# Optimization experiments

Measured on AMD Instinct MI355X. Metric: run time of the kernel, lower is better.

The kernel has to match this reference:

```python
import jax, jax.numpy as jnp
import numpy as np

EPS = 1e-10

def gru_dir(x, Wih, Whh, bih, bhh, reverse=False):
    # x: [B,T,in]; torch GRU gate order r,z,n
    B = x.shape[0]
    H = Whh.shape[1]
    xs = jnp.einsum('bti,gi->btg', x, Wih) + bih  # [B,T,3H] input proj precomputed
    if reverse:
        xs = xs[:, ::-1]
    h0 = jnp.zeros((B, H), x.dtype)
    def step(h, xt):
        gh = h @ Whh.T + bhh
        xr, xz, xn = jnp.split(xt, 3, axis=-1)
        hr, hz, hn = jnp.split(gh, 3, axis=-1)
        r = jax.nn.sigmoid(xr + hr)
        z = jax.nn.sigmoid(xz + hz)
        n = jnp.tanh(xn + r * hn)
        h = (1.0 - z) * n + z * h
        return h, h
    _, ys = jax.lax.scan(step, h0, jnp.swapaxes(xs, 0, 1))
    ys = jnp.swapaxes(ys, 0, 1)
    if reverse:
        ys = ys[:, ::-1]
    return ys

def bigru(x, Wih, Whh, bih, bhh):
    f = gru_dir(x, Wih[0], Whh[0], bih[0], bhh[0], False)
    b = gru_dir(x, Wih[1], Whh[1], bih[1], bhh[1], True)
    return jnp.concatenate([f, b], -1)

def graph_decomp(lab, nb, nb_mask, layers=2):
    # lab: [N,D]; nb: [N,K] neighbor ids; nb_mask: [N,K] 0/1 validity
    m = nb_mask.astype(lab.dtype)
    for _ in range(layers):
        Lj = lab[nb]                                   # [N,K,D]
        x1 = jnp.sum(lab[:, None, :] * Lj, -1)         # <Li,Lj>
        x2 = jnp.sum(Lj * Lj, -1) + EPS                # <Lj,Lj>
        proj = (x1 / x2)[..., None] * Lj               # scaled projection
        deg = jnp.sum(m, -1)                           # [N]
        mean = jnp.sum(proj * m[..., None], 1) / jnp.maximum(deg, 1.0)[:, None]
        lab = jnp.where(deg[:, None] > 0, lab - mean, lab)
    return lab

def code_wise(query, context):
    # query [B,N,D], context [B,T,D] -> [B,1,D]
    S = jnp.einsum('btd,bnd->btn', context, query)
    att = jax.nn.softmax(jnp.max(S, 2), axis=-1)       # [B,T]
    return jnp.einsum('bt,btd->bd', att, context)[:, None, :]

def mask_attention(query, context):
    # query [B,L,D], context [B,T,D] -> [B,T,D]
    att = jnp.einsum('btd,bld->btl', context, query)
    am = jnp.where(att == 0, -jnp.inf, att)
    sm = jax.nn.softmax(am, axis=-1)
    sm = jnp.where(jnp.isnan(sm), 0.0, sm)             # NaN rows (all -inf) -> 0
    return jnp.einsum('btl,bld->btd', sm, query)

def fact_separation(verdict_hidden, circ):
    scenario = mask_attention(verdict_hidden, circ)
    x3 = jnp.sum(circ * scenario, 2)
    x4 = jnp.sum(scenario * scenario, 2) + EPS
    similar = (x3 / x4)[..., None] * scenario
    return similar, circ - similar


def setup_inputs() -> dict:
    key = jax.random.key(0)
    ks = iter(jax.random.split(key, 64))
    def nrm(shape, s=0.1):
        return jax.random.normal(next(ks), shape, jnp.float32) * s
    def ints(shape, hi):
        return jax.random.randint(next(ks), shape, 0, hi)
    V, D, H = 339503, 200, 150
    B, T = 32, 512
    Nc, Na, K = 119, 103, 8
    Lc, La, Lv = 32, 64, 50
    def gru_p(pfx, din, h):
        return {pfx+'_Wih': nrm((2, 3*h, din)), pfx+'_Whh': nrm((2, 3*h, h)),
                pfx+'_bih': nrm((2, 3*h)), pfx+'_bhh': nrm((2, 3*h))}
    inp = {'emb': nrm((V, D), 1.0)}
    inp.update(gru_p('enc', D, H))
    inp.update(gru_p('encch', D, H))
    inp.update(gru_p('term', 6*H, 3*H))
    inp.update(gru_p('art', 8*H, 4*H))
    inp.update({'Wc': nrm((Nc, 6*H)), 'bc': nrm((Nc,)),
                'Wa': nrm((Na, 8*H)), 'ba': nrm((Na,)),
                'Wt': nrm((11, 6*H)), 'bt': nrm((11,))})
    inp.update({'documents': ints((B, T), V),
                'charge_tokens': ints((Nc, Lc), V),
                'article_tokens': ints((Na, La), V),
                'charge_nb': ints((Nc, K), Nc),
                'charge_nb_mask': ints((Nc, K), 2).astype(jnp.int32),
                'article_nb': ints((Na, K), Na),
                'article_nb_mask': ints((Na, K), 2).astype(jnp.int32),
                'verdict_charge_tokens': ints((Nc, Lv), V),
                'verdict_article_tokens': ints((Na, Lv), V)})
    return inp


def reference(emb, enc_Wih, enc_Whh, enc_bih, enc_bhh,
              encch_Wih, encch_Whh, encch_bih, encch_bhh,
              term_Wih, term_Whh, term_bih, term_bhh,
              art_Wih, art_Whh, art_bih, art_bhh,
              Wc, bc, Wa, ba, Wt, bt,
              documents, charge_tokens, article_tokens,
              charge_nb, charge_nb_mask, article_nb, article_nb_mask,
              verdict_charge_tokens, verdict_article_tokens):
    # label encodings (shared encoder_charge)
    ch = bigru(emb[charge_tokens], encch_Wih, encch_Whh, encch_bih, encch_bhh)
    ar = bigru(emb[article_tokens], encch_Wih, encch_Whh, encch_bih, encch_bhh)
    _charge = ch.mean(1); ori_a = _charge                      # [Nc,300]
    _article = ar.mean(1); ori_b = _article                    # [Na,300]
    new_charge = graph_decomp(_charge, charge_nb, charge_nb_mask, 2)
    new_article = graph_decomp(_article, article_nb, article_nb_mask, 2)

    d_hidden = bigru(emb[documents], enc_Wih, enc_Whh, enc_bih, enc_bhh)  # [B,T,300]
    B, T, Dh = d_hidden.shape
    def cw(labels):
        q = jnp.broadcast_to(labels[None], (B,) + labels.shape)
        return code_wise(q, d_hidden)                          # [B,1,300]
    tile = lambda v: jnp.broadcast_to(v, (B, T, Dh))

    d_hc = cw(new_charge); d_a = cw(ori_a)
    fact_charge = jnp.concatenate([d_hidden, tile(d_hc), tile(d_a)], -1)  # [B,T,900]
    charge_out = fact_charge.mean(1) @ Wc.T + bc
    cp = jnp.argmax(charge_out, 1)                             # predicted charge ids
    vch = bigru(emb[verdict_charge_tokens[cp]], enc_Wih, enc_Whh, enc_bih, enc_bhh)
    adc, sec = fact_separation(vch, d_hidden)

    d_ha = cw(new_article); d_b = cw(ori_b)
    fact_article = jnp.concatenate([d_hidden, tile(d_ha), adc, tile(d_b)], -1)  # [B,T,1200]
    fah = bigru(fact_article, art_Wih, art_Whh, art_bih, art_bhh).mean(1)
    article_out = fah @ Wa.T + ba
    ap = jnp.argmax(article_out, 1)
    var = bigru(emb[verdict_article_tokens[ap]], enc_Wih, enc_Whh, enc_bih, enc_bhh)
    ssc, dsc = fact_separation(var, sec)

    term = jnp.concatenate([d_hidden, ssc, dsc], -1)           # [B,T,900]
    th = bigru(term, term_Wih, term_Whh, term_bih, term_bhh).mean(1)
    time_out = th @ Wt.T + bt
    return charge_out, article_out, time_out
```

## Files before the change

kernel.cpp:

```cpp
#include <hip/hip_runtime.h>
#include <hip/hip_bf16.h>

#define DEVI __device__ __forceinline__

DEVI float sigm(float x){ return 1.f/(1.f+expf(-x)); }

typedef int v4i __attribute__((ext_vector_type(4)));
typedef float f4 __attribute__((ext_vector_type(4)));
using bf16x8 = __attribute__((ext_vector_type(8))) short;

DEVI v4i make_srsrc(const void* p, unsigned bytes){
  unsigned long long a = (unsigned long long)p;
  v4i r;
  r.x = (int)(a & 0xFFFFFFFFull);
  r.y = (int)((a >> 32) & 0xFFFFull);
  r.z = (int)bytes;
  r.w = 0x00020000;
  return r;
}

DEVI unsigned packsplit(float a){
  unsigned u = __float_as_uint(a);
  unsigned hi = (u + 0x7fffu + ((u >> 16) & 1u)) & 0xffff0000u;
  float res = a - __uint_as_float(hi);
  unsigned v = __float_as_uint(res);
  unsigned lo = ((v + 0x7fffu + ((v >> 16) & 1u)) >> 16) & 0xffffu;
  return hi | lo;
}

__global__ void k_transpose(const float* __restrict__ in, float* __restrict__ out, int R, int C){
  int b = blockIdx.y;
  long n = (long)R*C;
  long i = (long)blockIdx.x*256 + threadIdx.x;
  if (i < n){
    int r = (int)(i / C), c = (int)(i % C);
    out[(long)b*n + (long)c*R + r] = in[(long)b*n + i];
  }
}

__global__ void k_gather_p(const float* __restrict__ emb, const int* __restrict__ tok, unsigned* __restrict__ out){
  int row = blockIdx.x; int c = threadIdx.x;
  if (c < 200) out[(long)row*200 + c] = packsplit(emb[(long)tok[row]*200 + c]);
}
__global__ void k_gather_sel_p(const float* __restrict__ emb, const int* __restrict__ tok, const int* __restrict__ sel, unsigned* __restrict__ out){
  int t = blockIdx.x, b = blockIdx.y; int c = threadIdx.x;
  if (c < 200){
    int tk = tok[(long)sel[b]*50 + t];
    out[((long)b*50 + t)*200 + c] = packsplit(emb[(long)tk*200 + c]);
  }
}

__global__ void k_packAc(const float* __restrict__ src, unsigned* __restrict__ dst, long n){
  long i = (long)blockIdx.x*256 + threadIdx.x;
  if (i < n) dst[i] = packsplit(src[i]);
}
__global__ void k_packW(const float* __restrict__ src, unsigned* __restrict__ dst, int R, int K, int KP){
  long i = (long)blockIdx.x*256 + threadIdx.x;
  if (i < (long)R*KP){
    int r = (int)(i / KP), k = (int)(i % KP);
    dst[i] = (k < K) ? packsplit(src[(long)r*K + k]) : 0u;
  }
}

__global__ __launch_bounds__(256) void k_gemm_bf3(
    const unsigned* __restrict__ Ap, const unsigned* __restrict__ Wp,
    const float* __restrict__ bias, float* __restrict__ C,
    int M, int N, int K, int KP, long sW, long sC, long sBias)
{
  int dir = blockIdx.z;
  Wp += (long)dir*sW; C += (long)dir*sC;
  if (bias) bias += (long)dir*sBias;
  int n0 = blockIdx.x*128, m0 = blockIdx.y*128;
  __shared__ unsigned short Ah[128*72], Al[128*72], Bh[128*72], Bl[128*72];
  int tid = threadIdx.x;
  int w = tid >> 6, lane = tid & 63;
  int l15 = lane & 15, lg = lane >> 4;
  f4 acc[2][8] = {};

  for (int k0 = 0; k0 < K; k0 += 64){
    __syncthreads();
    for (int u = tid; u < 2048; u += 256){
      int r = u >> 4, q = u & 15;
      int k = k0 + q*4;
      uint4 pa = make_uint4(0,0,0,0);
      if (k + 4 <= K) pa = *(const uint4*)&Ap[(long)(m0 + r)*K + k];
      ushort4 h4, s4;
      h4.x=(unsigned short)(pa.x>>16); s4.x=(unsigned short)(pa.x&0xffff);
      h4.y=(unsigned short)(pa.y>>16); s4.y=(unsigned short)(pa.y&0xffff);
      h4.z=(unsigned short)(pa.z>>16); s4.z=(unsigned short)(pa.z&0xffff);
      h4.w=(unsigned short)(pa.w>>16); s4.w=(unsigned short)(pa.w&0xffff);
      *(ushort4*)&Ah[r*72 + q*4] = h4;
      *(ushort4*)&Al[r*72 + q*4] = s4;
      int n = n0 + r;
      uint4 pw = make_uint4(0,0,0,0);
      if (n < N && k + 4 <= KP) pw = *(const uint4*)&Wp[(long)n*KP + k];
      ushort4 wh, wl;
      wh.x=(unsigned short)(pw.x>>16); wl.x=(unsigned short)(pw.x&0xffff);
      wh.y=(unsigned short)(pw.y>>16); wl.y=(unsigned short)(pw.y&0xffff);
      wh.z=(unsigned short)(pw.z>>16); wl.z=(unsigned short)(pw.z&0xffff);
      wh.w=(unsigned short)(pw.w>>16); wl.w=(unsigned short)(pw.w&0xffff);
      *(ushort4*)&Bh[r*72 + q*4] = wh;
      *(ushort4*)&Bl[r*72 + q*4] = wl;
    }
    __syncthreads();
    bf16x8 ah[2][2], al[2][2];
    #pragma unroll
    for (int fm=0; fm<2; fm++)
      #pragma unroll
      for (int ks=0; ks<2; ks++){
        int idx = (w*32 + fm*16 + l15)*72 + ks*32 + lg*8;
        ah[fm][ks] = *(const bf16x8*)&Ah[idx];
        al[fm][ks] = *(const bf16x8*)&Al[idx];
      }
    #pragma unroll
    for (int fn=0; fn<8; fn++){
      int bidx0 = (fn*16 + l15)*72 + lg*8;
      bf16x8 bh0 = *(const bf16x8*)&Bh[bidx0];
      bf16x8 bh1 = *(const bf16x8*)&Bh[bidx0 + 32];
      bf16x8 bl0 = *(const bf16x8*)&Bl[bidx0];
      bf16x8 bl1 = *(const bf16x8*)&Bl[bidx0 + 32];
      #pragma unroll
      for (int fm=0; fm<2; fm++){
        f4 a = acc[fm][fn];
        a = __builtin_amdgcn_mfma_f32_16x16x32_bf16(ah[fm][0], bh0, a, 0, 0, 0);
        a = __builtin_amdgcn_mfma_f32_16x16x32_bf16(al[fm][0], bh0, a, 0, 0, 0);
        a = __builtin_amdgcn_mfma_f32_16x16x32_bf16(ah[fm][0], bl0, a, 0, 0, 0);
        a = __builtin_amdgcn_mfma_f32_16x16x32_bf16(ah[fm][1], bh1, a, 0, 0, 0);
        a = __builtin_amdgcn_mfma_f32_16x16x32_bf16(al[fm][1], bh1, a, 0, 0, 0);
        a = __builtin_amdgcn_mfma_f32_16x16x32_bf16(ah[fm][1], bl1, a, 0, 0, 0);
        acc[fm][fn] = a;
      }
    }
  }
  #pragma unroll
  for (int fm=0; fm<2; fm++)
    #pragma unroll
    for (int fn=0; fn<8; fn++){
      int row = m0 + w*32 + fm*16 + lg*4;
      int col = n0 + fn*16 + l15;
      if (col < N){
        float bv = bias ? bias[col] : 0.f;
        #pragma unroll
        for (int r2=0; r2<4; r2++)
          if (row + r2 < M)
            C[(long)(row+r2)*N + col] = acc[fm][fn][r2] + bv;
      }
    }
}

__global__ __launch_bounds__(256) void k_gemm128(
    const float* __restrict__ A, const float* __restrict__ W,
    const float* __restrict__ bias, float* __restrict__ C,
    int M, int N, int K, long sA, long sW, long sC, long sBias)
{
  int bz = blockIdx.z;
  A += (long)bz*sA; W += (long)bz*sW; C += (long)bz*sC;
  if (bias) bias += (long)bz*sBias;
  int n0 = blockIdx.x*128, m0 = blockIdx.y*128;
  __shared__ float As[16][132];
  __shared__ float Bs[16][132];
  int tid = threadIdx.x;
  int tx = tid & 15, ty = tid >> 4;
  float acc[8][8] = {};
  const bool k4 = ((K & 3) == 0);
  for (int k0 = 0; k0 < K; k0 += 16){
    #pragma unroll
    for (int half = 0; half < 2; half++){
      int s = tid + half*256;
      int r = s >> 2;
      int kq = (s & 3) << 2;
      int k = k0 + kq;
      int m = m0 + r;
      float4 va = make_float4(0.f,0.f,0.f,0.f);
      if (m < M){
        if (k4 && k + 3 < K) va = *(const float4*)&A[(long)m*K + k];
        else {
          float* pv = (float*)&va;
          #pragma unroll
          for (int u=0; u<4; u++) if (k+u < K) pv[u] = A[(long)m*K + k + u];
        }
      }
      As[kq+0][r]=va.x; As[kq+1][r]=va.y; As[kq+2][r]=va.z; As[kq+3][r]=va.w;
      int n = n0 + r;
      float4 vb = make_float4(0.f,0.f,0.f,0.f);
      if (n < N){
        if (k4 && k + 3 < K) vb = *(const float4*)&W[(long)n*K + k];
        else {
          float* pv = (float*)&vb;
          #pragma unroll
          for (int u=0; u<4; u++) if (k+u < K) pv[u] = W[(long)n*K + k + u];
        }
      }
      Bs[kq+0][r]=vb.x; Bs[kq+1][r]=vb.y; Bs[kq+2][r]=vb.z; Bs[kq+3][r]=vb.w;
    }
    __syncthreads();
    #pragma unroll
    for (int kk=0;kk<16;kk++){
      float a[8], b[8];
      *(float4*)&a[0] = *(const float4*)&As[kk][ty*8];
      *(float4*)&a[4] = *(const float4*)&As[kk][ty*8+4];
      *(float4*)&b[0] = *(const float4*)&Bs[kk][tx*8];
      *(float4*)&b[4] = *(const float4*)&Bs[kk][tx*8+4];
      #pragma unroll
      for (int i=0;i<8;i++)
        #pragma unroll
        for (int j=0;j<8;j++)
          acc[i][j] += a[i]*b[j];
    }
    __syncthreads();
  }
  #pragma unroll
  for (int i=0;i<8;i++){
    int m = m0 + ty*8 + i;
    if (m >= M) continue;
    #pragma unroll
    for (int j=0;j<8;j++){
      int n = n0 + tx*8 + j;
      if (n < N) C[(long)m*N + n] = acc[i][j] + (bias ? bias[n] : 0.f);
    }
  }
}

__global__ __launch_bounds__(512) void k_gru_small(
    const float* __restrict__ xs, long xsDir,
    const float* __restrict__ Wt, const float* __restrict__ bhh,
    float* __restrict__ y, int yld,
    float* __restrict__ meanOut, int meanld,
    int T)
{
  int item = blockIdx.x, dir = blockIdx.y;
  const float* xsd = xs + (long)dir*xsDir + (long)item*T*450;
  const float* Wtd = Wt + (long)dir*150*450;
  int tid = threadIdx.x;
  float bh = (tid < 450) ? bhh[(long)dir*450 + tid] : 0.f;
  __shared__ float hs[152];
  __shared__ float gs[456];
  if (tid < 150) hs[tid] = 0.f;
  float hsum = 0.f;
  __syncthreads();
  for (int t=0;t<T;t++){
    int tt = dir ? (T-1-t) : t;
    if (tid < 450){
      float g = bh;
      const float* wp = Wtd + tid;
      #pragma unroll 15
      for (int k=0;k<150;k++) g += hs[k] * wp[(long)k*450];
      gs[tid] = g;
    }
    __syncthreads();
    if (tid < 150){
      const float* xr = xsd + (long)tt*450;
      float r = sigm(xr[tid]     + gs[tid]);
      float z = sigm(xr[150+tid] + gs[150+tid]);
      float nn = tanhf(xr[300+tid] + r*gs[300+tid]);
      float h = (1.f-z)*nn + z*hs[tid];
      hs[tid] = h;
      hsum += h;
      if (y) y[((long)item*T + tt)*yld + dir*150 + tid] = h;
    }
    __syncthreads();
  }
  if (meanOut && tid < 150)
    meanOut[(long)item*meanld + dir*150 + tid] = hsum / (float)T;
}

#define GDOT(AC, W, A) AC += W.x*A.x + W.y*A.y + W.z*A.z + W.w*A.w;
template<int H, int HS, int LDW, int HPAD, int KL, int NCB>
__global__ __launch_bounds__(256) void k_gru_persist(
    const float* __restrict__ xs, long xsDir,
    const float* __restrict__ Whh, const float* __restrict__ bhh,
    float* hA, float* hB,
    float* __restrict__ ysum, int ysld,
    int T, int* flags, int* go)
{
  constexpr int H3 = 3*H;
  constexpr int CPR = HS/4;
  constexpr int NCH = 16*CPR;
  constexpr int NIT = (NCH + 255)/256;
  int wid = blockIdx.x;
  int dir = wid / (2*NCB);
  int rem = wid % (2*NCB);
  int bb  = rem / NCB;
  int cb  = rem % NCB;
  int quad = dir*2 + bb;
  int qbase = quad*64;
  int c0  = cb*10;
  int tid = threadIdx.x;

  const float* xsd = xs + (long)dir*xsDir;
  const float* Wd  = Whh + (long)dir*(long)H*H3;
  const float* bhd = bhh + (long)dir*H3;

  __shared__ float hs[16*HPAD];
  __shared__ float Wl[30*LDW];
  __shared__ float blds[32];
  __shared__ float gl[30*16];
  __shared__ float part[240*12];

  for (int u = tid; u < 30*HS; u += 256){
    int r = u / HS, k = u % HS;
    long row = (long)(r/10)*H + c0 + (r%10);
    Wl[r*LDW + k] = (k < H) ? Wd[row*H + k] : 0.f;
  }
  if (tid < 30) blds[tid] = bhd[(long)(tid/10)*H + (c0 + tid%10)];

  int ks = tid / 40;
  int rem2 = tid % 40;
  int rg = rem2 / 4;
  int ig = rem2 % 4;
  bool alive = (tid < 240);
  int r0 = rg*3;
  int it0 = ig*4;
  int kbase = ks*KL;

  int uit = tid / 10, uci = tid % 10;
  int uc = c0 + uci;
  int ub = bb*16 + uit;
  float ysacc = 0.f;

  float xv0 = 0.f, xv1 = 0.f, xv2 = 0.f;
  if (tid < 160){
    int tt0 = dir ? (T-1) : 0;
    const float* xr = xsd + ((long)ub*T + tt0)*H3;
    xv0 = xr[uc]; xv1 = xr[H+uc]; xv2 = xr[2*H+uc];
  }

  __syncthreads();

  for (int t=0; t<T; t++){
    float* hp = ((t & 1) ? hB : hA) + (long)dir*32*HS;
    float* hn = ((t & 1) ? hA : hB) + (long)dir*32*HS;

    {
      v4i srsrc = make_srsrc(hp, 32u*HS*4u);
      f4 sbuf[NIT];
      #pragma unroll
      for (int i = 0; i < NIT; i++){
        int u = tid + i*256;
        if (u < NCH){
          int voff = ((bb*16 + u/CPR)*HS + (u%CPR)*4)*4;
          asm volatile("buffer_load_dwordx4 %0, %1, %2, 0 offen sc0 sc1"
                       : "=v"(sbuf[i]) : "v"(voff), "s"(srsrc));
        }
      }
      asm volatile("s_waitcnt vmcnt(0)" ::: "memory");
      __builtin_amdgcn_sched_barrier(0);
      #pragma unroll
      for (int i = 0; i < NIT; i++){
        int u = tid + i*256;
        if (u < NCH)
          *(f4*)&hs[(u/CPR)*HPAD + (u%CPR)*4] = sbuf[i];
      }
    }
    __syncthreads();

    if (alive){
      float acc[3][4];
      #pragma unroll
      for (int a=0;a<3;a++)
        #pragma unroll
        for (int b=0;b<4;b++) acc[a][b] = 0.f;
      const float* wr0 = &Wl[(r0+0)*LDW + kbase];
      const float* wr1 = &Wl[(r0+1)*LDW + kbase];
      const float* wr2 = &Wl[(r0+2)*LDW + kbase];
      const float* h0  = &hs[(it0+0)*HPAD + kbase];
      const float* h1  = &hs[(it0+1)*HPAD + kbase];
      const float* h2  = &hs[(it0+2)*HPAD + kbase];
      const float* h3  = &hs[(it0+3)*HPAD + kbase];
      for (int jq = 0; jq < KL; jq += 4){
        float4 w0 = *(const float4*)&wr0[jq];
        float4 w1 = *(const float4*)&wr1[jq];
        float4 w2 = *(const float4*)&wr2[jq];
        float4 a0 = *(const float4*)&h0[jq];
        float4 a1 = *(const float4*)&h1[jq];
        float4 a2 = *(const float4*)&h2[jq];
        float4 a3 = *(const float4*)&h3[jq];
        GDOT(acc[0][0], w0, a0) GDOT(acc[0][1], w0, a1) GDOT(acc[0][2], w0, a2) GDOT(acc[0][3], w0, a3)
        GDOT(acc[1][0], w1, a0) GDOT(acc[1][1], w1, a1) GDOT(acc[1][2], w1, a2) GDOT(acc[1][3], w1, a3)
        GDOT(acc[2][0], w2, a0) GDOT(acc[2][1], w2, a1) GDOT(acc[2][2], w2, a2) GDOT(acc[2][3], w2, a3)
      }
      #pragma unroll
      for (int a=0;a<3;a++)
        *(float4*)&part[tid*12 + a*4] = make_float4(acc[a][0],acc[a][1],acc[a][2],acc[a][3]);
    }
    __syncthreads();

    if (alive){
      #pragma unroll
      for (int vv=0; vv<2; vv++){
        int v = tid + vv*240;
        int row = v >> 4, item = v & 15;
        int base = ((row/3)*4 + (item>>2))*12 + (row%3)*4 + (item&3);
        float sum = blds[row];
        #pragma unroll
        for (int s=0; s<6; s++) sum += part[s*480 + base];
        gl[row*16 + item] = sum;
      }
    }
    __syncthreads();

    if (tid < 160){
      float r  = sigm(xv0 + gl[(uci)*16    + uit]);
      float z  = sigm(xv1 + gl[(10+uci)*16 + uit]);
      float nn = tanhf(xv2 + r*gl[(20+uci)*16 + uit]);
      float hv = hs[uit*HPAD + uc];
      float hne = (1.f-z)*nn + z*hv;
      __hip_atomic_store(&hn[(long)ub*HS + uc], hne, __ATOMIC_RELAXED, __HIP_MEMORY_SCOPE_AGENT);
      ysacc += hne;
    }
    __syncthreads();

    float nx0 = 0.f, nx1 = 0.f, nx2 = 0.f;
    if (tid < 160 && t+1 < T){
      int tt1 = dir ? (T-2-t) : (t+1);
      const float* xr = xsd + ((long)ub*T + tt1)*H3;
      nx0 = xr[uc]; nx1 = xr[H+uc]; nx2 = xr[2*H+uc];
    }

    if (t+1 < T){
      if (tid == 0)
        __hip_atomic_store(&flags[qbase + cb], t+1, __ATOMIC_RELAXED, __HIP_MEMORY_SCOPE_AGENT);
      if (cb == 0){
        if (tid < NCB){
          while (__hip_atomic_load(&flags[qbase + tid], __ATOMIC_RELAXED, __HIP_MEMORY_SCOPE_AGENT) < t+1)
            __builtin_amdgcn_s_sleep(2);
        }
        __syncthreads();
        if (tid == 0)
          __hip_atomic_store(&go[quad*32], t+1, __ATOMIC_RELAXED, __HIP_MEMORY_SCOPE_AGENT);
      } else {
        if (tid == 0){
          while (__hip_atomic_load(&go[quad*32], __ATOMIC_RELAXED, __HIP_MEMORY_SCOPE_AGENT) < t+1)
            __builtin_amdgcn_s_sleep(2);
        }
        __syncthreads();
      }
    }
    xv0 = nx0; xv1 = nx1; xv2 = nx2;
  }
  if (tid < 160)
    ysum[(long)ub*ysld + dir*H + uc] = ysacc;
}

__global__ __launch_bounds__(256) void k_graphdecomp(
   const float* __restrict__ labIn, float* __restrict__ labOut,
   const int* __restrict__ nb, const int* __restrict__ nbm, int N)
{
  int n = blockIdx.x; if (n >= N) return;
  int tid = threadIdx.x;
  __shared__ float ln[300];
  __shared__ float red[12];
  for (int d=tid; d<300; d+=256) ln[d] = labIn[(long)n*300+d];
  float deg = 0.f;
  for (int k=0;k<8;k++) deg += (float)nbm[n*8+k];
  float invdeg = 1.f / fmaxf(deg, 1.f);
  float acc0 = 0.f, acc1 = 0.f;
  __syncthreads();
  for (int k=0;k<8;k++){
    int j = nb[n*8+k];
    float mk = (float)nbm[n*8+k];
    const float* lj = labIn + (long)j*300;
    float p1=0.f, p2=0.f;
    for (int d=tid; d<300; d+=256){ float v = lj[d]; p1 += ln[d]*v; p2 += v*v; }
    for (int o=32;o>0;o>>=1){ p1 += __shfl_down(p1,o); p2 += __shfl_down(p2,o); }
    __syncthreads();
    int w = tid>>6, lane = tid&63;
    if (lane==0){ red[w]=p1; red[4+w]=p2; }
    __syncthreads();
    float x1 = red[0]+red[1]+red[2]+red[3];
    float x2 = red[4]+red[5]+red[6]+red[7];
    float coef = (x1 / (x2 + 1e-10f)) * mk * invdeg;
    acc0 += coef * lj[tid];
    if (tid + 256 < 300) acc1 += coef * lj[tid+256];
    __syncthreads();
  }
  bool pos = deg > 0.f;
  labOut[(long)n*300 + tid]                       = pos ? (ln[tid]     - acc0) : ln[tid];
  if (tid+256 < 300) labOut[(long)n*300 + tid+256] = pos ? (ln[tid+256] - acc1) : ln[tid+256];
}

__global__ void k_copy(const float* __restrict__ src, float* __restrict__ dst, long n){
  long i = (long)blockIdx.x*256+threadIdx.x; if (i<n) dst[i]=src[i];
}

__global__ void k_cw_rowmax(const float* __restrict__ S, float* __restrict__ Mv){
  const int ofs[4]={0,119,238,341};
  const int wid[4]={119,119,103,103};
  int s = blockIdx.y; int row = blockIdx.x*256+threadIdx.x;
  if (row < 16384){
    const float* p = S + (long)row*444 + ofs[s];
    float m = -3.4e38f;
    int w = wid[s];
    for (int n=0;n<w;n++) m = fmaxf(m, p[n]);
    Mv[(long)s*16384+row] = m;
  }
}
__global__ void k_cw_softmax(const float* __restrict__ Mv, float* __restrict__ att){
  int b=blockIdx.x, s=blockIdx.y, tid=threadIdx.x;
  const float* src = Mv + (long)s*16384 + (long)b*512;
  __shared__ float red[256];
  float v0 = src[tid], v1 = src[tid+256];
  red[tid] = fmaxf(v0,v1); __syncthreads();
  for (int o=128;o>0;o>>=1){ if (tid<o) red[tid]=fmaxf(red[tid],red[tid+o]); __syncthreads(); }
  float m = red[0]; __syncthreads();
  float e0=expf(v0-m), e1=expf(v1-m);
  red[tid]=e0+e1; __syncthreads();
  for (int o=128;o>0;o>>=1){ if (tid<o) red[tid]+=red[tid+o]; __syncthreads(); }
  float inv = 1.f/red[0];
  float* dst = att + ((long)s*32 + b)*512;
  dst[tid]=e0*inv; dst[tid+256]=e1*inv;
}
__global__ void k_cw_out(const float* __restrict__ att, const float* __restrict__ DH, float* __restrict__ outp){
  int b=blockIdx.x, s=blockIdx.y, tid=threadIdx.x;
  __shared__ float a[512];
  for (int i=tid;i<512;i+=256) a[i]=att[((long)s*32+b)*512+i];
  __syncthreads();
  for (int d=tid; d<300; d+=256){
    float acc=0.f;
    for (int t=0;t<512;t++) acc += a[t]*DH[((long)b*512+t)*300+d];
    outp[((long)s*32+b)*300+d]=acc;
  }
}

__global__ void k_masksm(float* __restrict__ att, long nrows){
  long row = (long)blockIdx.x*256 + threadIdx.x;
  if (row >= nrows) return;
  float* p = att + row*50;
  float m = -INFINITY;
  for (int l=0;l<50;l++){ float a = p[l]; if (a != 0.f && a > m) m = a; }
  if (m == -INFINITY){ for (int l=0;l<50;l++) p[l] = 0.f; return; }
  float s = 0.f;
  for (int l=0;l<50;l++){ float a = p[l]; float e = (a==0.f) ? 0.f : expf(a-m); p[l]=e; s+=e; }
  float inv = 1.f/s;
  for (int l=0;l<50;l++) p[l] *= inv;
}

__global__ void k_factsep(const float* circ, const float* scen,
                          float* simOut, float* diffOut, long nrows)
{
  int lane = threadIdx.x & 63;
  long row = (long)blockIdx.x*4 + (threadIdx.x >> 6);
  if (row >= nrows) return;
  const float* c = circ + row*300;
  const float* s = scen + row*300;
  float x3=0.f, x4=0.f;
  for (int d=lane; d<300; d+=64){ float sv=s[d]; x3 += c[d]*sv; x4 += sv*sv; }
  for (int o=32;o>0;o>>=1){ x3 += __shfl_down(x3,o); x4 += __shfl_down(x4,o); }
  x3 = __shfl(x3,0); x4 = __shfl(x4,0);
  float coef = x3 / (x4 + 1e-10f);
  for (int d=lane; d<300; d+=64){
    float sv = s[d]; float cv = c[d];
    float sim = coef*sv;
    simOut[row*300+d] = sim;
    diffOut[row*300+d] = cv - sim;
  }
}

__global__ void k_factart_p(const float* __restrict__ DH, const float* __restrict__ dha,
                            const float* __restrict__ adc, const float* __restrict__ db,
                            unsigned* __restrict__ out)
{
  long row = blockIdx.x; int b = (int)(row >> 9);
  for (int c=threadIdx.x; c<1200; c+=256){
    float v;
    if (c < 300) v = DH[row*300 + c];
    else if (c < 600) v = dha[(long)b*300 + (c-300)];
    else if (c < 900) v = adc[row*300 + (c-600)];
    else v = db[(long)b*300 + (c-900)];
    out[row*1200 + c] = packsplit(v);
  }
}
__global__ void k_termcat_p(const float* __restrict__ DH, const float* __restrict__ ssc,
                            const float* __restrict__ dsc, unsigned* __restrict__ out){
  long row = blockIdx.x;
  for (int c=threadIdx.x; c<900; c+=256){
    float v = (c<300) ? DH[row*300+c] : (c<600 ? ssc[row*300+(c-300)] : dsc[row*300+(c-600)]);
    out[row*900+c] = packsplit(v);
  }
}

__global__ __launch_bounds__(256) void k_classify(
    const float* __restrict__ s0, const float* __restrict__ s1, const float* __restrict__ s2,
    int L, int Kf, float scale,
    const float* __restrict__ W, const float* __restrict__ bias, int N,
    float* __restrict__ out, int* __restrict__ amax)
{
  int b = blockIdx.x; int tid = threadIdx.x;
  __shared__ float feat[1200];
  __shared__ float logit[128];
  for (int i=tid; i<Kf; i+=256){
    int seg = i / L, c = i % L;
    const float* s = (seg==0) ? s0 : (seg==1 ? s1 : s2);
    feat[i] = s[(long)b*L + c] * scale;
  }
  __syncthreads();
  for (int n=tid; n<N; n+=256){
    float acc = bias[n];
    const float* w = W + (long)n*Kf;
    for (int k=0;k<Kf;k++) acc += feat[k]*w[k];
    out[(long)b*N + n] = acc;
    logit[n] = acc;
  }
  __syncthreads();
  if (amax && tid==0){
    float best = logit[0]; int bi=0;
    for (int n=1;n<N;n++) if (logit[n] > best){ best=logit[n]; bi=n; }
    amax[b] = bi;
  }
}

static inline int cdiv(long a, long b){ return (int)((a + b - 1)/b); }

extern "C" void kernel_launch(void* const* d_in, const int* in_sizes, int n_in,
                              void* d_out, int out_size, void* d_ws, size_t ws_size,
                              hipStream_t stream)
{
  (void)in_sizes; (void)n_in; (void)out_size;
  const float* emb     = (const float*)d_in[0];
  const float* encWih  = (const float*)d_in[1];
  const float* encWhh  = (const float*)d_in[2];
  const float* encbih  = (const float*)d_in[3];
  const float* encbhh  = (const float*)d_in[4];
  const float* cchWih  = (const float*)d_in[5];
  const float* cchWhh  = (const float*)d_in[6];
  const float* cchbih  = (const float*)d_in[7];
  const float* cchbhh  = (const float*)d_in[8];
  const float* termWih = (const float*)d_in[9];
  const float* termWhh = (const float*)d_in[10];
  const float* termbih = (const float*)d_in[11];
  const float* termbhh = (const float*)d_in[12];
  const float* artWih  = (const float*)d_in[13];
  const float* artWhh  = (const float*)d_in[14];
  const float* artbih  = (const float*)d_in[15];
  const float* artbhh  = (const float*)d_in[16];
  const float* Wc      = (const float*)d_in[17];
  const float* bc      = (const float*)d_in[18];
  const float* Wa      = (const float*)d_in[19];
  const float* ba      = (const float*)d_in[20];
  const float* Wt_     = (const float*)d_in[21];
  const float* bt_     = (const float*)d_in[22];
  const int* docs    = (const int*)d_in[23];
  const int* chtok   = (const int*)d_in[24];
  const int* artok   = (const int*)d_in[25];
  const int* chnb    = (const int*)d_in[26];
  const int* chnbm   = (const int*)d_in[27];
  const int* arnb    = (const int*)d_in[28];
  const int* arnbm   = (const int*)d_in[29];
  const int* vchtok  = (const int*)d_in[30];
  const int* vartok  = (const int*)d_in[31];
  float* ob = (float*)d_out;
  float* ws = (float*)d_ws;

  constexpr long O_WTENC = 0;
  constexpr long O_WTCCH = O_WTENC + 135000;
  constexpr long O_WTART = O_WTCCH + 135000;
  constexpr long O_WTTERM= O_WTART + 2160000;
  constexpr long O_DH    = O_WTTERM + 1215000;
  constexpr long O_DMEAN = O_DH + 4915200;
  constexpr long O_CHM   = O_DMEAN + 9600;
  constexpr long O_ARM   = O_CHM + 35700;
  constexpr long O_LAB   = O_ARM + 30900;
  constexpr long O_GDT   = O_LAB + 133200;
  constexpr long O_CWM   = O_GDT + 35700;
  constexpr long O_CWA   = O_CWM + 65536;
  constexpr long O_CWO   = O_CWA + 65536;
  constexpr long O_CP    = O_CWO + 38400;
  constexpr long O_VCH   = O_CP + 64;
  constexpr long O_VCHT  = O_VCH + 480000;
  constexpr long O_ATT   = O_VCHT + 480000;
  constexpr long O_SCEN  = O_ATT + 819200;
  constexpr long O_ADC   = O_SCEN + 4915200;
  constexpr long O_SEC   = O_ADC + 4915200;
  constexpr long O_HBUF  = O_SEC + 4915200;
  constexpr long O_YSUM  = O_HBUF + 76800;
  constexpr long O_GATH  = O_YSUM + 38400;
  constexpr long O_XSS   = O_GATH + 3276800;
  constexpr long O_PF    = O_XSS + 5932800;
  constexpr long O_XB    = O_PF + 19660800;
  constexpr long TOTAL   = O_XB + 58982400;
  if (ws_size < (size_t)TOTAL * 4) return;

  float* WT_ENC = ws + O_WTENC;
  float* WT_CCH = ws + O_WTCCH;
  unsigned* PWENC = (unsigned*)(ws + O_WTART);
  unsigned* PWCCH = (unsigned*)(ws + O_WTTERM);
  float* DH     = ws + O_DH;
  float* DMEAN  = ws + O_DMEAN;
  float* CHM    = ws + O_CHM;
  float* ARM    = ws + O_ARM;
  float* LAB    = ws + O_LAB;
  float* GDT    = ws + O_GDT;
  float* CWM    = ws + O_CWM;
  float* CWA    = ws + O_CWA;
  float* CWO    = ws + O_CWO;
  int*   CP     = (int*)(ws + O_CP);
  int*   AP     = CP + 32;
  float* VCH    = ws + O_VCH;
  float* VCHT   = ws + O_VCHT;
  float* ATT    = ws + O_ATT;
  float* SCEN   = ws + O_SCEN;
  float* ADC    = ws + O_ADC;
  float* SEC    = ws + O_SEC;
  float* HBUF   = ws + O_HBUF;
  float* YSUM   = ws + O_YSUM;
  float* GATH   = ws + O_GATH;
  float* XSS    = ws + O_XSS;
  float* PF     = ws + O_PF;
  float* XB     = ws + O_XB;
  int*   FLAGS  = (int*)GDT;
  int*   GO     = FLAGS + 256;

  k_transpose<<<dim3(cdiv(450L*150,256),2),256,0,stream>>>(encWhh, WT_ENC, 450,150);
  k_transpose<<<dim3(cdiv(450L*150,256),2),256,0,stream>>>(cchWhh, WT_CCH, 450,150);
  k_packW<<<cdiv(900L*208,256),256,0,stream>>>(encWih, PWENC, 900, 200, 208);
  k_packW<<<cdiv(900L*208,256),256,0,stream>>>(cchWih, PWCCH, 900, 200, 208);

  k_gather_p<<<3808,256,0,stream>>>(emb, chtok, (unsigned*)GATH);
  k_gemm_bf3<<<dim3(4,cdiv(3808,128),2),256,0,stream>>>((const unsigned*)GATH, PWCCH,
      cchbih, XSS, 3808, 450, 200, 208, 450L*208, 3808L*450, 450);
  k_gru_small<<<dim3(119,2),512,0,stream>>>(XSS, 3808L*450, WT_CCH, cchbhh,
      nullptr,0, CHM,300, 32);

  k_gather_p<<<6592,256,0,stream>>>(emb, artok, (unsigned*)GATH);
  k_gemm_bf3<<<dim3(4,cdiv(6592,128),2),256,0,stream>>>((const unsigned*)GATH, PWCCH,
      cchbih, XSS, 6592, 450, 200, 208, 450L*208, 6592L*450, 450);
  k_gru_small<<<dim3(103,2),512,0,stream>>>(XSS, 6592L*450, WT_CCH, cchbhh,
      nullptr,0, ARM,300, 64);

  k_copy<<<cdiv(35700,256),256,0,stream>>>(CHM, LAB + 119L*300, 35700);
  k_copy<<<cdiv(30900,256),256,0,stream>>>(ARM, LAB + 341L*300, 30900);
  k_graphdecomp<<<119,256,0,stream>>>(CHM, GDT, chnb, chnbm, 119);
  k_graphdecomp<<<119,256,0,stream>>>(GDT, LAB, chnb, chnbm, 119);
  k_graphdecomp<<<103,256,0,stream>>>(ARM, GDT, arnb, arnbm, 103);
  k_graphdecomp<<<103,256,0,stream>>>(GDT, LAB + 238L*300, arnb, arnbm, 103);

  k_gather_p<<<16384,256,0,stream>>>(emb, docs, (unsigned*)GATH);
  k_gemm_bf3<<<dim3(4,128,2),256,0,stream>>>((const unsigned*)GATH, PWENC,
      encbih, PF, 16384, 450, 200, 208, 450L*208, 16384L*450, 450);
  k_gru_small<<<dim3(32,2),512,0,stream>>>(PF, 16384L*450, WT_ENC, encbhh,
      DH,300, DMEAN,300, 512);

  k_packAc<<<cdiv(16384L*300,256),256,0,stream>>>(DH, (unsigned*)XB, 16384L*300);
  k_packW<<<cdiv(444L*304,256),256,0,stream>>>(LAB, (unsigned*)XB + 16384L*300, 444, 300, 304);
  k_gemm_bf3<<<dim3(4,128,1),256,0,stream>>>((const unsigned*)XB, (const unsigned*)XB + 16384L*300,
      nullptr, PF, 16384, 444, 300, 304, 0, 0, 0);
  k_cw_rowmax<<<dim3(64,4),256,0,stream>>>(PF, CWM);
  k_cw_softmax<<<dim3(32,4),256,0,stream>>>(CWM, CWA);
  k_cw_out<<<dim3(32,4),256,0,stream>>>(CWA, DH, CWO);

  k_classify<<<32,256,0,stream>>>(DMEAN, CWO, CWO + 32L*300,
      300, 900, 1.f, Wc, bc, 119, ob, CP);

  k_gather_sel_p<<<dim3(50,32),256,0,stream>>>(emb, vchtok, CP, (unsigned*)GATH);
  k_gemm_bf3<<<dim3(4,13,2),256,0,stream>>>((const unsigned*)GATH, PWENC,
      encbih, XSS, 1600, 450, 200, 208, 450L*208, 1600L*450, 450);
  k_gru_small<<<dim3(32,2),512,0,stream>>>(XSS, 1600L*450, WT_ENC, encbhh,
      VCH,300, nullptr,0, 50);

  k_gemm128<<<dim3(1,4,32),256,0,stream>>>(DH, VCH, nullptr, ATT,
      512,50,300, 512L*300, 50L*300, 512L*50, 0);
  k_masksm<<<64,256,0,stream>>>(ATT, 16384);
  k_transpose<<<dim3(cdiv(15000,256),32),256,0,stream>>>(VCH, VCHT, 50, 300);
  k_gemm128<<<dim3(3,4,32),256,0,stream>>>(ATT, VCHT, nullptr, SCEN,
      512,300,50, 512L*50, 300L*50, 512L*300, 0);
  k_factsep<<<4096,256,0,stream>>>(DH, SCEN, ADC, SEC, 16384);

  k_factart_p<<<16384,256,0,stream>>>(DH, CWO + 2L*32*300, ADC, CWO + 3L*32*300, (unsigned*)PF);
  k_packW<<<cdiv(2L*1800*1216,256),256,0,stream>>>(artWih, (unsigned*)XSS, 2*1800, 1200, 1216);
  k_gemm_bf3<<<dim3(15,128,2),256,0,stream>>>((const unsigned*)PF, (const unsigned*)XSS,
      artbih, XB, 16384, 1800, 1200, 1216, 1800L*1216, 16384L*1800, 1800);
  hipMemsetAsync(FLAGS, 0, 512*sizeof(int), stream);
  hipMemsetAsync(HBUF, 0, 76800*sizeof(float), stream);
  k_gru_persist<600,600,604,604,100,60><<<240,256,0,stream>>>(
      XB, 16384L*1800, artWhh, artbhh, HBUF, HBUF+38400, YSUM, 1200, 512, FLAGS, GO);
  k_classify<<<32,256,0,stream>>>(YSUM, nullptr, nullptr,
      1200, 1200, 1.f/512.f, Wa, ba, 103, ob + 3808, AP);

  k_gather_sel_p<<<dim3(50,32),256,0,stream>>>(emb, vartok, AP, (unsigned*)GATH);
  k_gemm_bf3<<<dim3(4,13,2),256,0,stream>>>((const unsigned*)GATH, PWENC,
      encbih, XSS, 1600, 450, 200, 208, 450L*208, 1600L*450, 450);
  k_gru_small<<<dim3(32,2),512,0,stream>>>(XSS, 1600L*450, WT_ENC, encbhh,
      VCH,300, nullptr,0, 50);

  k_gemm128<<<dim3(1,4,32),256,0,stream>>>(SEC, VCH, nullptr, ATT,
      512,50,300, 512L*300, 50L*300, 512L*50, 0);
  k_masksm<<<64,256,0,stream>>>(ATT, 16384);
  k_transpose<<<dim3(cdiv(15000,256),32),256,0,stream>>>(VCH, VCHT, 50, 300);
  k_gemm128<<<dim3(3,4,32),256,0,stream>>>(ATT, VCHT, nullptr, SCEN,
      512,300,50, 512L*50, 300L*50, 512L*300, 0);
  k_factsep<<<4096,256,0,stream>>>(SEC, SCEN, SCEN, SEC, 16384);

  k_termcat_p<<<16384,256,0,stream>>>(DH, SCEN, SEC, (unsigned*)PF);
  k_packW<<<cdiv(2L*1350*912,256),256,0,stream>>>(termWih, (unsigned*)GATH, 2*1350, 900, 912);
  k_gemm_bf3<<<dim3(11,128,2),256,0,stream>>>((const unsigned*)PF, (const unsigned*)GATH,
      termbih, XB, 16384, 1350, 900, 912, 1350L*912, 16384L*1350, 1350);
  hipMemsetAsync(FLAGS, 0, 512*sizeof(int), stream);
  hipMemsetAsync(HBUF, 0, 76800*sizeof(float), stream);
  k_gru_persist<450,456,460,460,76,45><<<180,256,0,stream>>>(
      XB, 16384L*1350, termWhh, termbhh, HBUF, HBUF+29184, YSUM, 900, 512, FLAGS, GO);
  k_classify<<<32,256,0,stream>>>(YSUM, nullptr, nullptr,
      900, 900, 1.f/512.f, Wt_, bt_, 11, ob + 7104, nullptr);
}
```

Before: 12.21 ms.

## Use split-bf16 MFMA for recurrent matvec in persistent GRU kernel

Replaces the FP32 FMA dot-product tiling and cross-thread partial-sum reduction in the persistent GRU step with split-bf16 (hi/lo) MFMA 16x16x32 on two waves, storing weights and hidden state as bf16 hi/lo pairs in LDS. It also keeps the previous hidden value in a register instead of rereading LDS. The aim is to cut per-timestep latency on the serial recurrence by removing the partial buffer and one barrier. The cost is packing h into bf16 halves every step, a three-term split that drops the lo*lo term, and only two of four waves doing compute.

```diff
diff --git a/kernel.cpp b/kernel.cpp
--- a/kernel.cpp
+++ b/kernel.cpp
@@ -264,8 +264,7 @@
     meanOut[(long)item*meanld + dir*150 + tid] = hsum / (float)T;
 }
 
-#define GDOT(AC, W, A) AC += W.x*A.x + W.y*A.y + W.z*A.z + W.w*A.w;
-template<int H, int HS, int LDW, int HPAD, int KL, int NCB>
+template<int H, int HS, int KM, int SW, int NCB>
 __global__ __launch_bounds__(256) void k_gru_persist(
     const float* __restrict__ xs, long xsDir,
     const float* __restrict__ Whh, const float* __restrict__ bhh,
@@ -277,6 +276,7 @@
   constexpr int CPR = HS/4;
   constexpr int NCH = 16*CPR;
   constexpr int NIT = (NCH + 255)/256;
+  constexpr int NK  = KM/32;
   int wid = blockIdx.x;
   int dir = wid / (2*NCB);
   int rem = wid % (2*NCB);
@@ -286,36 +286,36 @@
   int qbase = quad*64;
   int c0  = cb*10;
   int tid = threadIdx.x;
+  int w = tid >> 6, lane = tid & 63;
+  int l15 = lane & 15, lg = lane >> 4;
 
   const float* xsd = xs + (long)dir*xsDir;
   const float* Wd  = Whh + (long)dir*(long)H*H3;
   const float* bhd = bhh + (long)dir*H3;
 
-  __shared__ float hs[16*HPAD];
-  __shared__ float Wl[30*LDW];
+  __shared__ unsigned short Wh[32*SW], Wlo[32*SW];
+  __shared__ unsigned short Hh[16*SW], Hl[16*SW];
   __shared__ float blds[32];
   __shared__ float gl[30*16];
-  __shared__ float part[240*12];
-
-  for (int u = tid; u < 30*HS; u += 256){
-    int r = u / HS, k = u % HS;
-    long row = (long)(r/10)*H + c0 + (r%10);
-    Wl[r*LDW + k] = (k < H) ? Wd[row*H + k] : 0.f;
+
+  for (int u = tid; u < 32*KM; u += 256){
+    int r = u / KM, k = u % KM;
+    float val = 0.f;
+    if (r < 30 && k < H) val = Wd[((long)(r/10)*H + c0 + (r%10))*H + k];
+    unsigned ps = packsplit(val);
+    Wh[r*SW + k]  = (unsigned short)(ps >> 16);
+    Wlo[r*SW + k] = (unsigned short)(ps & 0xffffu);
   }
   if (tid < 30) blds[tid] = bhd[(long)(tid/10)*H + (c0 + tid%10)];
-
-  int ks = tid / 40;
-  int rem2 = tid % 40;
-  int rg = rem2 / 4;
-  int ig = rem2 % 4;
-  bool alive = (tid < 240);
-  int r0 = rg*3;
-  int it0 = ig*4;
-  int kbase = ks*KL;
+  for (int u = tid; u < 16*(KM-HS); u += 256){
+    int item = u / (KM-HS), k = HS + u % (KM-HS);
+    Hh[item*SW + k] = 0; Hl[item*SW + k] = 0;
+  }
 
   int uit = tid / 10, uci = tid % 10;
   int uc = c0 + uci;
   int ub = bb*16 + uit;
+  float hreg = 0.f;
   float ysacc = 0.f;
 
   float xv0 = 0.f, xv1 = 0.f, xv2 = 0.f;
@@ -348,64 +348,57 @@
       #pragma unroll
       for (int i = 0; i < NIT; i++){
         int u = tid + i*256;
-        if (u < NCH)
-          *(f4*)&hs[(u/CPR)*HPAD + (u%CPR)*4] = sbuf[i];
-      }
-    }
-    __syncthreads();
-
-    if (alive){
-      float acc[3][4];
+        if (u < NCH){
+          int item = u / CPR;
+          int k = (u % CPR)*4;
+          unsigned p0 = packsplit(sbuf[i][0]);
+          unsigned p1 = packsplit(sbuf[i][1]);
+          unsigned p2 = packsplit(sbuf[i][2]);
+          unsigned p3 = packsplit(sbuf[i][3]);
+          ushort4 h4 = make_ushort4((unsigned short)(p0>>16), (unsigned short)(p1>>16),
+                                    (unsigned short)(p2>>16), (unsigned short)(p3>>16));
+          ushort4 l4 = make_ushort4((unsigned short)(p0&0xffffu), (unsigned short)(p1&0xffffu),
+                                    (unsigned short)(p2&0xffffu), (unsigned short)(p3&0xffffu));
+          *(ushort4*)&Hh[item*SW + k] = h4;
+          *(ushort4*)&Hl[item*SW + k] = l4;
+        }
+      }
+    }
+    __syncthreads();
+
+    if (w < 2){
+      f4 acc = {0.f, 0.f, 0.f, 0.f};
+      const int arow = (w*16 + l15)*SW;
+      const int brow = l15*SW;
       #pragma unroll
-      for (int a=0;a<3;a++)
-        #pragma unroll
-        for (int b=0;b<4;b++) acc[a][b] = 0.f;
-      const float* wr0 = &Wl[(r0+0)*LDW + kbase];
-      const float* wr1 = &Wl[(r0+1)*LDW + kbase];
-      const float* wr2 = &Wl[(r0+2)*LDW + kbase];
-      const float* h0  = &hs[(it0+0)*HPAD + kbase];
-      const float* h1  = &hs[(it0+1)*HPAD + kbase];
-      const float* h2  = &hs[(it0+2)*HPAD + kbase];
-      const float* h3  = &hs[(it0+3)*HPAD + kbase];
-      for (int jq = 0; jq < KL; jq += 4){
-        float4 w0 = *(const float4*)&wr0[jq];
-        float4 w1 = *(const float4*)&wr1[jq];
-        float4 w2 = *(const float4*)&wr2[jq];
-        float4 a0 = *(const float4*)&h0[jq];
-        float4 a1 = *(const float4*)&h1[jq];
-        float4 a2 = *(const float4*)&h2[jq];
-        float4 a3 = *(const float4*)&h3[jq];
-        GDOT(acc[0][0], w0, a0) GDOT(acc[0][1], w0, a1) GDOT(acc[0][2], w0, a2) GDOT(acc[0][3], w0, a3)
-        GDOT(acc[1][0], w1, a0) GDOT(acc[1][1], w1, a1) GDOT(acc[1][2], w1, a2) GDOT(acc[1][3], w1, a3)
-        GDOT(acc[2][0], w2, a0) GDOT(acc[2][1], w2, a1) GDOT(acc[2][2], w2, a2) GDOT(acc[2][3], w2, a3)
+      for (int kk = 0; kk < NK; kk++){
+        int kb = kk*32 + lg*8;
+        bf16x8 a_h = *(const bf16x8*)&Wh[arow + kb];
+        bf16x8 a_l = *(const bf16x8*)&Wlo[arow + kb];
+        bf16x8 b_h = *(const bf16x8*)&Hh[brow + kb];
+        bf16x8 b_l = *(const bf16x8*)&Hl[brow + kb];
+        acc = __builtin_amdgcn_mfma_f32_16x16x32_bf16(a_h, b_h, acc, 0, 0, 0);
+        acc = __builtin_amdgcn_mfma_f32_16x16x32_bf16(a_l, b_h, acc, 0, 0, 0);
+        acc = __builtin_amdgcn_mfma_f32_16x16x32_bf16(a_h, b_l, acc, 0, 0, 0);
       }
       #pragma unroll
-      for (int a=0;a<3;a++)
-        *(float4*)&part[tid*12 + a*4] = make_float4(acc[a][0],acc[a][1],acc[a][2],acc[a][3]);
-    }
-    __syncthreads();
-
-    if (alive){
-      #pragma unroll
-      for (int vv=0; vv<2; vv++){
-        int v = tid + vv*240;
-        int row = v >> 4, item = v & 15;
-        int base = ((row/3)*4 + (item>>2))*12 + (row%3)*4 + (item&3);
-        float sum = blds[row];
-        #pragma unroll
-        for (int s=0; s<6; s++) sum += part[s*480 + base];
-        gl[row*16 + item] = sum;
+      for (int r2 = 0; r2 < 4; r2++){
+        int row = w*16 + lg*4 + r2;
+        if (row < 30) gl[row*16 + l15] = acc[r2];
       }
     }
     __syncthreads();
 
     if (tid < 160){
-      float r  = sigm(xv0 + gl[(uci)*16    + uit]);
-      float z  = sigm(xv1 + gl[(10+uci)*16 + uit]);
-      float nn = tanhf(xv2 + r*gl[(20+uci)*16 + uit]);
-      float hv = hs[uit*HPAD + uc];
-      float hne = (1.f-z)*nn + z*hv;
+      float gr = gl[uci*16      + uit] + blds[uci];
+      float gz = gl[(10+uci)*16 + uit] + blds[10+uci];
+      float gn = gl[(20+uci)*16 + uit] + blds[20+uci];
+      float r  = sigm(xv0 + gr);
+      float z  = sigm(xv1 + gz);
+      float nn = tanhf(xv2 + r*gn);
+      float hne = (1.f-z)*nn + z*hreg;
       __hip_atomic_store(&hn[(long)ub*HS + uc], hne, __ATOMIC_RELAXED, __HIP_MEMORY_SCOPE_AGENT);
+      hreg = hne;
       ysacc += hne;
     }
     __syncthreads();
@@ -771,7 +764,7 @@
       artbih, XB, 16384, 1800, 1200, 1216, 1800L*1216, 16384L*1800, 1800);
   hipMemsetAsync(FLAGS, 0, 512*sizeof(int), stream);
   hipMemsetAsync(HBUF, 0, 76800*sizeof(float), stream);
-  k_gru_persist<600,600,604,604,100,60><<<240,256,0,stream>>>(
+  k_gru_persist<600,600,608,616,60><<<240,256,0,stream>>>(
       XB, 16384L*1800, artWhh, artbhh, HBUF, HBUF+38400, YSUM, 1200, 512, FLAGS, GO);
   k_classify<<<32,256,0,stream>>>(YSUM, nullptr, nullptr,
       1200, 1200, 1.f/512.f, Wa, ba, 103, ob + 3808, AP);
@@ -796,7 +789,7 @@
       termbih, XB, 16384, 1350, 900, 912, 1350L*912, 16384L*1350, 1350);
   hipMemsetAsync(FLAGS, 0, 512*sizeof(int), stream);
   hipMemsetAsync(HBUF, 0, 76800*sizeof(float), stream);
-  k_gru_persist<450,456,460,460,76,45><<<180,256,0,stream>>>(
+  k_gru_persist<450,456,480,488,45><<<180,256,0,stream>>>(
       XB, 16384L*1350, termWhh, termbhh, HBUF, HBUF+29184, YSUM, 900, 512, FLAGS, GO);
   k_classify<<<32,256,0,stream>>>(YSUM, nullptr, nullptr,
       900, 900, 1.f/512.f, Wt_, bt_, 11, ob + 7104, nullptr);
```

Result: faster. 9.904 ms (-18.9%).
